# Performance work log

Measured on AMD Instinct MI355X. Metric: run time of the kernel, lower is better.

Reference implementation:

```python
import jax, jax.numpy as jnp
import numpy as np

N, D = 8192, 512


def setup_inputs() -> dict:
    key = jax.random.key(0)
    ks = jax.random.split(key, 4)
    scale = 1.0 / np.sqrt(D)
    x = jax.random.normal(ks[0], (N, D), dtype=jnp.float32)
    Wq = jax.random.normal(ks[1], (D, D), dtype=jnp.float32) * scale
    Wk = jax.random.normal(ks[2], (D, D), dtype=jnp.float32) * scale
    Wv = jax.random.normal(ks[3], (D, D), dtype=jnp.float32) * scale
    bq = jnp.zeros((D,), dtype=jnp.float32)
    bk = jnp.zeros((D,), dtype=jnp.float32)
    bv = jnp.zeros((D,), dtype=jnp.float32)
    # causal additive mask: 0 on/below diagonal, -1e9 above
    mask = jnp.where(jnp.arange(N)[:, None] >= jnp.arange(N)[None, :], 0.0, -1e9).astype(jnp.float32)
    return {"x": x, "mask": mask, "Wq": Wq, "bq": bq, "Wk": Wk, "bk": bk, "Wv": Wv, "bv": bv}


def reference(x, mask, Wq, bq, Wk, bk, Wv, bv):
    # torch Linear: y = x @ W.T + b
    q = x @ Wq.T + bq  # [N, D]
    k = x @ Wk.T + bk  # [N, D]
    v = x @ Wv.T + bv  # [N, D]
    inv_sqrt_d = 1.0 / jnp.sqrt(jnp.asarray(D, dtype=x.dtype))
    scores = q @ k.T * inv_sqrt_d + mask          # [N, N] -- the HBM-heavy intermediate
    attention = jax.nn.softmax(scores, axis=-1)   # softmax over key axis
    weighted = attention @ v                       # [N, D]
    return weighted
```

## Files before the change

### kernel.cpp

```cpp
#include <hip/hip_runtime.h>
#include <hip/hip_bf16.h>
#include <stdint.h>


#define N_TOK 8192
#define DIM   512
#define NQB   128
#define CCH   12
#define MAXCH 11
#define NCHTOT 748

typedef __attribute__((ext_vector_type(8))) short bfrag;
typedef __attribute__((ext_vector_type(4))) float facc;
typedef __attribute__((ext_vector_type(4))) unsigned short us4v;
typedef __attribute__((ext_vector_type(2))) float f32x2v;

#define MFMA16(a, b, c) __builtin_amdgcn_mfma_f32_16x16x32_bf16((a), (b), (c), 0, 0, 0)

__device__ __forceinline__ unsigned short f2bf(float f) {
    union { float f; unsigned int u; } v; v.f = f;
    unsigned int r = v.u + 0x7fffu + ((v.u >> 16) & 1u);
    return (unsigned short)(r >> 16);
}
__device__ __forceinline__ float bf2f(unsigned int bits16) {
    union { unsigned int u; float f; } v; v.u = bits16 << 16;
    return v.f;
}
__device__ __forceinline__ void cp16(const unsigned short* g, unsigned short* l) {
    __builtin_amdgcn_global_load_lds(
        (const __attribute__((address_space(1))) void*)g,
        (__attribute__((address_space(3))) void*)l, 16, 0, 0);
}

__device__ __forceinline__ int part_idx(int qb, int c) {
    return qb + 122 * c - 6 * c * c;
}

__global__ void cvt_x_kernel(const float* __restrict__ src,
                             unsigned short* __restrict__ dst, int n4) {
    int i = blockIdx.x * blockDim.x + threadIdx.x;
    if (i >= n4) return;
    float4 v = ((const float4*)src)[i];
    us4v o; o[0] = f2bf(v.x); o[1] = f2bf(v.y); o[2] = f2bf(v.z); o[3] = f2bf(v.w);
    ((us4v*)dst)[i] = o;
}

__global__ void cvt_w_kernel(const float* __restrict__ wq,
                             const float* __restrict__ wk,
                             const float* __restrict__ wv,
                             unsigned short* __restrict__ dst) {
    int i = blockIdx.x * blockDim.x + threadIdx.x;
    int g = i >> 16;
    int o = i & 65535;
    const float* s = (g == 0) ? wq : (g == 1) ? wk : wv;
    float4 v = ((const float4*)s)[o];
    us4v p; p[0] = f2bf(v.x); p[1] = f2bf(v.y); p[2] = f2bf(v.z); p[3] = f2bf(v.w);
    ((us4v*)dst)[i] = p;
}

__global__ __launch_bounds__(256) void qkv_gemm(
    const unsigned short* __restrict__ xb,
    const unsigned short* __restrict__ wb,
    const float* __restrict__ biasq, const float* __restrict__ biask,
    const float* __restrict__ biasv,
    unsigned short* __restrict__ Qb, unsigned short* __restrict__ Kb,
    unsigned short* __restrict__ VTb) {
    const int z    = blockIdx.z;
    const int lane = threadIdx.x & 63;
    const int wv   = threadIdx.x >> 6;
    const int r0   = blockIdx.x * 128 + wv * 32;
    const int c0   = blockIdx.y * 64;
    const unsigned short* w = wb + z * 262144;
    const float* bias = (z == 0) ? biasq : (z == 1) ? biask : biasv;
    const int lr  = lane & 15;
    const int lkc = lane >> 4;
    const int lk  = lkc * 8;

    facc acc[2][4] = {};
    const unsigned short* ap0 = xb + (size_t)(r0 + lr) * 512 + lk;
    const unsigned short* bp0 = w  + (size_t)(c0 + lr) * 512 + lk;

#pragma unroll
    for (int s = 0; s < 16; ++s) {
        const int kk = s * 32;
        bfrag a0 = *(const bfrag*)(ap0 + kk);
        bfrag a1 = *(const bfrag*)(ap0 + 16 * 512 + kk);
        bfrag b0 = *(const bfrag*)(bp0 + kk);
        bfrag b1 = *(const bfrag*)(bp0 + 16 * 512 + kk);
        bfrag b2 = *(const bfrag*)(bp0 + 32 * 512 + kk);
        bfrag b3 = *(const bfrag*)(bp0 + 48 * 512 + kk);
        acc[0][0] = MFMA16(a0, b0, acc[0][0]);
        acc[0][1] = MFMA16(a0, b1, acc[0][1]);
        acc[0][2] = MFMA16(a0, b2, acc[0][2]);
        acc[0][3] = MFMA16(a0, b3, acc[0][3]);
        acc[1][0] = MFMA16(a1, b0, acc[1][0]);
        acc[1][1] = MFMA16(a1, b1, acc[1][1]);
        acc[1][2] = MFMA16(a1, b2, acc[1][2]);
        acc[1][3] = MFMA16(a1, b3, acc[1][3]);
    }

    const int rbase = lkc * 4;
    if (z < 2) {
        unsigned short* out = (z == 0) ? Qb : Kb;
#pragma unroll
        for (int i = 0; i < 2; ++i)
#pragma unroll
            for (int j = 0; j < 4; ++j) {
                const int col = c0 + j * 16 + lr;
                const float bv_ = bias[col];
#pragma unroll
                for (int r = 0; r < 4; ++r) {
                    const int row = r0 + i * 16 + rbase + r;
                    out[(size_t)row * 512 + col] = f2bf(acc[i][j][r] + bv_);
                }
            }
    } else {
#pragma unroll
        for (int i = 0; i < 2; ++i)
#pragma unroll
            for (int j = 0; j < 4; ++j) {
                const int col = c0 + j * 16 + lr;
                const float bv_ = bias[col];
                us4v pk;
#pragma unroll
                for (int r = 0; r < 4; ++r) pk[r] = f2bf(acc[i][j][r] + bv_);
                *(us4v*)(VTb + (size_t)col * 8192 + (r0 + i * 16 + rbase)) = pk;
            }
    }
}

__global__ __launch_bounds__(512, 2) void attn_partial(
    const unsigned short* __restrict__ Qb, const unsigned short* __restrict__ Kb,
    const unsigned short* __restrict__ VTb,
    unsigned short* __restrict__ Opart, float* __restrict__ ml) {
    const int hb   = blockIdx.x;
    const int xcd  = hb & 7, pos = hb >> 3;
    const int idx  = (xcd < 4 ? xcd * 94 : 376 + (xcd - 4) * 93) + pos;
    int c = 0;
#pragma unroll
    for (int cc = 1; cc < MAXCH; ++cc)
        if (idx >= 134 * cc - 6 * cc * cc) c = cc;
    const int qb  = 12 * c + (idx - (134 * c - 6 * c * c));
    const int kb0 = c * CCH;
    const int kb1 = min(kb0 + CCH, qb + 1);

    const int tid  = threadIdx.x;
    const int lane = tid & 63;
    const int wv   = tid >> 6;
    const int sr   = wv & 3;
    const int ch   = wv >> 2;
    const int lr   = lane & 15;
    const int lkc  = lane >> 4;
    const int lk   = lkc * 8;
    const int qrow0 = qb * 64;

    __shared__ unsigned short Klds[2][64 * 512];
    __shared__ float          S_lds[64][65];
    __shared__ unsigned short P_lds[64][72];
    __shared__ float m_lds[64], l_lds[64], sc_lds[64];

    if (tid < 64) { m_lds[tid] = -1e30f; l_lds[tid] = 0.f; }

    auto stage_k = [&](int kb, int buf) {
        const unsigned short* src = Kb + (size_t)kb * (64 * 512) + (lane ^ wv) * 8;
#pragma unroll
        for (int i = 0; i < 8; ++i) {
            const int rl = wv + 8 * i;
            cp16(src + (size_t)rl * 512, &Klds[buf][rl * 512]);
        }
    };

    bfrag q[16];
    {
        const unsigned short* qp = Qb + (size_t)(qrow0 + sr * 16 + lr) * 512 + lk;
#pragma unroll
        for (int s = 0; s < 16; ++s) q[s] = *(const bfrag*)(qp + s * 32);
    }
    facc o[4][4] = {};
    stage_k(kb0, 0);
    __syncthreads();

    const int row = tid >> 3;
    const int sub = tid & 7;
    const float sm_scale = 0.044194173824159216f;
    int cur = 0;

    for (int kb = kb0; kb < kb1; ++kb) {
        const int cb = kb * 64;
        if (kb + 1 < kb1) stage_k(kb + 1, cur ^ 1);
        bfrag vbf[2][4];
#pragma unroll
        for (int s = 0; s < 2; ++s)
#pragma unroll
            for (int j = 0; j < 4; ++j)
                vbf[s][j] = *(const bfrag*)(VTb + (size_t)(wv * 64 + j * 16 + lr) * 8192
                                            + cb + s * 32 + lk);
#pragma unroll
        for (int tc = 0; tc < 2; ++tc) {
            facc sacc = {};
            const int rl = ch * 32 + tc * 16 + lr;
            const unsigned short* kbase = &Klds[cur][rl * 512];
            const int rx = rl & 7;
#pragma unroll
            for (int s = 0; s < 16; ++s) {
                const int slot = (s * 4 + lkc) ^ rx;
                bfrag bf = *(const bfrag*)(kbase + slot * 8);
                sacc = MFMA16(q[s], bf, sacc);
            }
#pragma unroll
            for (int r = 0; r < 4; ++r)
                S_lds[sr * 16 + lkc * 4 + r][ch * 32 + tc * 16 + lr] = sacc[r];
        }
        __syncthreads();

        {
            const int grow  = qrow0 + row;
            const bool diag = (kb == qb);
            float sv[8];
#pragma unroll
            for (int j = 0; j < 8; ++j) {
                float v = S_lds[row][sub * 8 + j] * sm_scale;
                if (diag && (cb + sub * 8 + j > grow)) v = -1e30f;
                sv[j] = v;
            }
            float mx = sv[0];
#pragma unroll
            for (int j = 1; j < 8; ++j) mx = fmaxf(mx, sv[j]);
            mx = fmaxf(mx, __shfl_xor(mx, 1));
            mx = fmaxf(mx, __shfl_xor(mx, 2));
            mx = fmaxf(mx, __shfl_xor(mx, 4));
            const float m_old = m_lds[row];
            const float m_new = fmaxf(m_old, mx);
            float sum = 0.f;
            bfrag pv_;
#pragma unroll
            for (int j = 0; j < 8; ++j) {
                float p = __expf(sv[j] - m_new);
                sum += p;
                pv_[j] = (short)f2bf(p);
            }
            sum += __shfl_xor(sum, 1);
            sum += __shfl_xor(sum, 2);
            sum += __shfl_xor(sum, 4);
            if (sub == 0) {
                const float scl = __expf(m_old - m_new);
                sc_lds[row] = scl;
                m_lds[row]  = m_new;
                l_lds[row]  = l_lds[row] * scl + sum;
            }
            *(bfrag*)(&P_lds[row][sub * 8]) = pv_;
        }
        __syncthreads();

#pragma unroll
        for (int i = 0; i < 4; ++i) {
            float s0 = sc_lds[i * 16 + lkc * 4 + 0];
            float s1 = sc_lds[i * 16 + lkc * 4 + 1];
            float s2 = sc_lds[i * 16 + lkc * 4 + 2];
            float s3 = sc_lds[i * 16 + lkc * 4 + 3];
#pragma unroll
            for (int j = 0; j < 4; ++j) {
                o[i][j][0] *= s0; o[i][j][1] *= s1;
                o[i][j][2] *= s2; o[i][j][3] *= s3;
            }
        }
#pragma unroll
        for (int s = 0; s < 2; ++s) {
            bfrag pa[4];
#pragma unroll
            for (int i = 0; i < 4; ++i)
                pa[i] = *(const bfrag*)(&P_lds[i * 16 + lr][s * 32 + lk]);
#pragma unroll
            for (int i = 0; i < 4; ++i)
#pragma unroll
                for (int j = 0; j < 4; ++j)
                    o[i][j] = MFMA16(pa[i], vbf[s][j], o[i][j]);
        }
        __syncthreads();
        cur ^= 1;
    }

    {
        const size_t obase = (size_t)idx * (64 * 512);
#pragma unroll
        for (int i = 0; i < 4; ++i)
#pragma unroll
            for (int j = 0; j < 4; ++j) {
                const int colb = wv * 64 + j * 16 + lr;
#pragma unroll
                for (int r = 0; r < 4; ++r) {
                    const int rrow = i * 16 + lkc * 4 + r;
                    Opart[obase + (size_t)rrow * 512 + colb] = f2bf(o[i][j][r]);
                }
            }
        if (tid < 64) {
            ml[(size_t)idx * 128 + tid * 2 + 0] = m_lds[tid];
            ml[(size_t)idx * 128 + tid * 2 + 1] = l_lds[tid];
        }
    }
}

__global__ __launch_bounds__(256) void combine_k(
    const unsigned short* __restrict__ Opart, const float* __restrict__ ml,
    float* __restrict__ out) {
    const int qb  = blockIdx.x;
    const int rg  = blockIdx.y;
    const int nch = qb / 12 + 1;
    const int tid = threadIdx.x;
    __shared__ float wts[MAXCH][8];

    if (tid < 8) {
        const int lrow = rg * 8 + tid;
        float M = -1e30f;
        for (int cc = 0; cc < nch; ++cc)
            M = fmaxf(M, ml[(size_t)part_idx(qb, cc) * 128 + lrow * 2]);
        float den = 0.f;
        for (int cc = 0; cc < nch; ++cc) {
            float mc = ml[(size_t)part_idx(qb, cc) * 128 + lrow * 2];
            float lc = ml[(size_t)part_idx(qb, cc) * 128 + lrow * 2 + 1];
            den += lc * __expf(mc - M);
        }
        const float inv = 1.f / den;
#pragma unroll
        for (int cc = 0; cc < MAXCH; ++cc)
            wts[cc][tid] = (cc < nch)
                ? __expf(ml[(size_t)part_idx(qb, cc) * 128 + lrow * 2] - M) * inv
                : 0.f;
    }
    __syncthreads();

    float a0[8] = {}, a1[8] = {};
#pragma unroll
    for (int cc = 0; cc < MAXCH; ++cc) {
        const size_t base = (size_t)part_idx(qb, cc) * (64 * 512);
#pragma unroll
        for (int r = 0; r < 8; ++r) {
            const unsigned int pk = *(const unsigned int*)(
                Opart + base + (size_t)(rg * 8 + r) * 512 + tid * 2);
            const float w = wts[cc][r];
            a0[r] += w * bf2f(pk & 0xffffu);
            a1[r] += w * bf2f(pk >> 16);
        }
    }
#pragma unroll
    for (int r = 0; r < 8; ++r) {
        f32x2v res; res[0] = a0[r]; res[1] = a1[r];
        *(f32x2v*)(out + (size_t)(qb * 64 + rg * 8 + r) * 512 + tid * 2) = res;
    }
}

extern "C" void kernel_launch(void* const* d_in, const int* in_sizes, int n_in,
                              void* d_out, int out_size, void* d_ws, size_t ws_size,
                              hipStream_t stream) {
    const float* x  = (const float*)d_in[0];
    const float* Wq = (const float*)d_in[2];
    const float* bq = (const float*)d_in[3];
    const float* Wk = (const float*)d_in[4];
    const float* bk = (const float*)d_in[5];
    const float* Wv = (const float*)d_in[6];
    const float* bv = (const float*)d_in[7];
    float* out = (float*)d_out;

    char* ws = (char*)d_ws;
    unsigned short* xb  = (unsigned short*)(ws);
    unsigned short* Wb  = (unsigned short*)(ws + 8388608);
    unsigned short* Qb  = (unsigned short*)(ws + 9961472);
    unsigned short* Kb  = (unsigned short*)(ws + 18350080);
    unsigned short* VTb = (unsigned short*)(ws + 26738688);
    unsigned short* Op  = (unsigned short*)(ws + 35127296);
    float*          mlp = (float*)(ws + 84148224);

    hipLaunchKernelGGL(cvt_x_kernel, dim3(4096), dim3(256), 0, stream, x, xb, 1048576);
    hipLaunchKernelGGL(cvt_w_kernel, dim3(768), dim3(256), 0, stream, Wq, Wk, Wv, Wb);
    hipLaunchKernelGGL(qkv_gemm, dim3(64, 8, 3), dim3(256), 0, stream,
                       xb, Wb, bq, bk, bv, Qb, Kb, VTb);
    hipLaunchKernelGGL(attn_partial, dim3(NCHTOT), dim3(512), 0, stream,
                       Qb, Kb, VTb, Op, mlp);
    hipLaunchKernelGGL(combine_k, dim3(NQB, 8), dim3(256), 0, stream, Op, mlp, out);
}
```

Before: 537.8 us.

## Tile QKV GEMM through double-buffered LDS, split QK accumulators, drop trailing barrier

```diff
diff --git a/kernel.cpp b/kernel.cpp
--- a/kernel.cpp
+++ b/kernel.cpp
@@ -26,7 +26,7 @@
     union { unsigned int u; float f; } v; v.u = bits16 << 16;
     return v.f;
 }
-__device__ __forceinline__ void cp16(const unsigned short* g, unsigned short* l) {
+__device__ __forceinline__ void cp16(const unsigned short* g, const unsigned short* l) {
     __builtin_amdgcn_global_load_lds(
         (const __attribute__((address_space(1))) void*)g,
         (__attribute__((address_space(3))) void*)l, 16, 0, 0);
@@ -58,7 +58,7 @@
     ((us4v*)dst)[i] = p;
 }
 
-__global__ __launch_bounds__(256) void qkv_gemm(
+__global__ __launch_bounds__(256, 2) void qkv_gemm(
     const unsigned short* __restrict__ xb,
     const unsigned short* __restrict__ wb,
     const float* __restrict__ biasq, const float* __restrict__ biask,
@@ -66,65 +66,91 @@
     unsigned short* __restrict__ Qb, unsigned short* __restrict__ Kb,
     unsigned short* __restrict__ VTb) {
     const int z    = blockIdx.z;
-    const int lane = threadIdx.x & 63;
-    const int wv   = threadIdx.x >> 6;
-    const int r0   = blockIdx.x * 128 + wv * 32;
-    const int c0   = blockIdx.y * 64;
-    const unsigned short* w = wb + z * 262144;
+    const int tid  = threadIdx.x;
+    const int lane = tid & 63;
+    const int w    = tid >> 6;
+    const int wr   = w >> 1, wc = w & 1;
+    const int r0   = blockIdx.x * 128;
+    const int c0   = blockIdx.y * 128;
+    const unsigned short* wmat = wb + z * 262144;
     const float* bias = (z == 0) ? biasq : (z == 1) ? biask : biasv;
     const int lr  = lane & 15;
     const int lkc = lane >> 4;
-    const int lk  = lkc * 8;
-
-    facc acc[2][4] = {};
-    const unsigned short* ap0 = xb + (size_t)(r0 + lr) * 512 + lk;
-    const unsigned short* bp0 = w  + (size_t)(c0 + lr) * 512 + lk;
-
-#pragma unroll
-    for (int s = 0; s < 16; ++s) {
-        const int kk = s * 32;
-        bfrag a0 = *(const bfrag*)(ap0 + kk);
-        bfrag a1 = *(const bfrag*)(ap0 + 16 * 512 + kk);
-        bfrag b0 = *(const bfrag*)(bp0 + kk);
-        bfrag b1 = *(const bfrag*)(bp0 + 16 * 512 + kk);
-        bfrag b2 = *(const bfrag*)(bp0 + 32 * 512 + kk);
-        bfrag b3 = *(const bfrag*)(bp0 + 48 * 512 + kk);
-        acc[0][0] = MFMA16(a0, b0, acc[0][0]);
-        acc[0][1] = MFMA16(a0, b1, acc[0][1]);
-        acc[0][2] = MFMA16(a0, b2, acc[0][2]);
-        acc[0][3] = MFMA16(a0, b3, acc[0][3]);
-        acc[1][0] = MFMA16(a1, b0, acc[1][0]);
-        acc[1][1] = MFMA16(a1, b1, acc[1][1]);
-        acc[1][2] = MFMA16(a1, b2, acc[1][2]);
-        acc[1][3] = MFMA16(a1, b3, acc[1][3]);
-    }
-
-    const int rbase = lkc * 4;
+
+    __shared__ unsigned short AB[2][2][128 * 64];
+
+    const int st_row = w * 8 + (lane >> 3);
+    const int st_gs  = ((lane & 7) ^ (lane >> 3)) * 8;
+    auto stage = [&](int step, int buf) {
+        const int kb = step * 64;
+#pragma unroll
+        for (int i = 0; i < 4; ++i) {
+            const int r = i * 32 + st_row;
+            cp16(xb   + (size_t)(r0 + r) * 512 + kb + st_gs,
+                 &AB[0][buf][(i * 256 + w * 64) * 8]);
+            cp16(wmat + (size_t)(c0 + r) * 512 + kb + st_gs,
+                 &AB[1][buf][(i * 256 + w * 64) * 8]);
+        }
+    };
+
+    facc acc[4][4] = {};
+    stage(0, 0);
+    __syncthreads();
+
+    int buf = 0;
+    for (int step = 0; step < 8; ++step) {
+        if (step + 1 < 8) stage(step + 1, buf ^ 1);
+        bfrag af[4][2], bf4[4][2];
+#pragma unroll
+        for (int i = 0; i < 4; ++i) {
+            const int m = wr * 64 + i * 16 + lr;
+            const int mb = m * 64, m7 = m & 7;
+            af[i][0] = *(const bfrag*)&AB[0][buf][mb + ((lkc) ^ m7) * 8];
+            af[i][1] = *(const bfrag*)&AB[0][buf][mb + ((4 + lkc) ^ m7) * 8];
+        }
+#pragma unroll
+        for (int j = 0; j < 4; ++j) {
+            const int n = wc * 64 + j * 16 + lr;
+            const int nb = n * 64, n7 = n & 7;
+            bf4[j][0] = *(const bfrag*)&AB[1][buf][nb + ((lkc) ^ n7) * 8];
+            bf4[j][1] = *(const bfrag*)&AB[1][buf][nb + ((4 + lkc) ^ n7) * 8];
+        }
+#pragma unroll
+        for (int kk = 0; kk < 2; ++kk)
+#pragma unroll
+            for (int i = 0; i < 4; ++i)
+#pragma unroll
+                for (int j = 0; j < 4; ++j)
+                    acc[i][j] = MFMA16(af[i][kk], bf4[j][kk], acc[i][j]);
+        __syncthreads();
+        buf ^= 1;
+    }
+
     if (z < 2) {
         unsigned short* out = (z == 0) ? Qb : Kb;
 #pragma unroll
-        for (int i = 0; i < 2; ++i)
+        for (int i = 0; i < 4; ++i)
 #pragma unroll
             for (int j = 0; j < 4; ++j) {
-                const int col = c0 + j * 16 + lr;
+                const int col = c0 + wc * 64 + j * 16 + lr;
                 const float bv_ = bias[col];
 #pragma unroll
                 for (int r = 0; r < 4; ++r) {
-                    const int row = r0 + i * 16 + rbase + r;
+                    const int row = r0 + wr * 64 + i * 16 + lkc * 4 + r;
                     out[(size_t)row * 512 + col] = f2bf(acc[i][j][r] + bv_);
                 }
             }
     } else {
 #pragma unroll
-        for (int i = 0; i < 2; ++i)
+        for (int i = 0; i < 4; ++i)
 #pragma unroll
             for (int j = 0; j < 4; ++j) {
-                const int col = c0 + j * 16 + lr;
+                const int col = c0 + wc * 64 + j * 16 + lr;
                 const float bv_ = bias[col];
                 us4v pk;
 #pragma unroll
                 for (int r = 0; r < 4; ++r) pk[r] = f2bf(acc[i][j][r] + bv_);
-                *(us4v*)(VTb + (size_t)col * 8192 + (r0 + i * 16 + rbase)) = pk;
+                *(us4v*)(VTb + (size_t)col * 8192 + (r0 + wr * 64 + i * 16 + lkc * 4)) = pk;
             }
     }
 }
@@ -197,19 +223,20 @@
                                             + cb + s * 32 + lk);
 #pragma unroll
         for (int tc = 0; tc < 2; ++tc) {
-            facc sacc = {};
+            facc sa0 = {}, sa1 = {};
             const int rl = ch * 32 + tc * 16 + lr;
             const unsigned short* kbase = &Klds[cur][rl * 512];
             const int rx = rl & 7;
 #pragma unroll
-            for (int s = 0; s < 16; ++s) {
-                const int slot = (s * 4 + lkc) ^ rx;
-                bfrag bf = *(const bfrag*)(kbase + slot * 8);
-                sacc = MFMA16(q[s], bf, sacc);
+            for (int s = 0; s < 16; s += 2) {
+                const int sl0 = (s * 4 + lkc) ^ rx;
+                const int sl1 = ((s + 1) * 4 + lkc) ^ rx;
+                sa0 = MFMA16(q[s],     *(const bfrag*)(kbase + sl0 * 8), sa0);
+                sa1 = MFMA16(q[s + 1], *(const bfrag*)(kbase + sl1 * 8), sa1);
             }
 #pragma unroll
             for (int r = 0; r < 4; ++r)
-                S_lds[sr * 16 + lkc * 4 + r][ch * 32 + tc * 16 + lr] = sacc[r];
+                S_lds[sr * 16 + lkc * 4 + r][ch * 32 + tc * 16 + lr] = sa0[r] + sa1[r];
         }
         __syncthreads();
 
@@ -276,7 +303,6 @@
                 for (int j = 0; j < 4; ++j)
                     o[i][j] = MFMA16(pa[i], vbf[s][j], o[i][j]);
         }
-        __syncthreads();
         cur ^= 1;
     }
 
@@ -372,7 +398,7 @@
 
     hipLaunchKernelGGL(cvt_x_kernel, dim3(4096), dim3(256), 0, stream, x, xb, 1048576);
     hipLaunchKernelGGL(cvt_w_kernel, dim3(768), dim3(256), 0, stream, Wq, Wk, Wv, Wb);
-    hipLaunchKernelGGL(qkv_gemm, dim3(64, 8, 3), dim3(256), 0, stream,
+    hipLaunchKernelGGL(qkv_gemm, dim3(64, 4, 3), dim3(256), 0, stream,
                        xb, Wb, bq, bk, bv, Qb, Kb, VTb);
     hipLaunchKernelGGL(attn_partial, dim3(NCHTOT), dim3(512), 0, stream,
                        Qb, Kb, VTb, Op, mlp);
```

Result: faster. 478.5 us (-11.0%).
